# Optimization experiments

Measured on AMD Instinct MI355X. Metric: run time of the kernel, lower is better.

The kernel has to match this reference:

```python
import jax, jax.numpy as jnp
import numpy as np

B, L, EMB, U, V = 128, 64, 512, 1024, 50257
BN_EPS = 0.001


def setup_inputs() -> dict:
    key = jax.random.key(0)
    ks = jax.random.split(key, 20)
    s = 0.02
    return {
        "x": jax.random.randint(ks[0], (B, 1), 0, V, dtype=jnp.int64),
        "features": jax.random.normal(ks[1], (B, L, EMB), jnp.float32),
        "hidden": jax.random.normal(ks[2], (1, B, U), jnp.float32),
        "emb_table": jax.random.normal(ks[3], (V, EMB), jnp.float32) * s,
        "Uattn_w": jax.random.normal(ks[4], (U, EMB), jnp.float32) * s,
        "Uattn_b": jnp.zeros((U,), jnp.float32),
        "Wattn_w": jax.random.normal(ks[5], (U, U), jnp.float32) * s,
        "Wattn_b": jnp.zeros((U,), jnp.float32),
        "Vattn_w": jax.random.normal(ks[6], (1, U), jnp.float32) * s,
        "Vattn_b": jnp.zeros((1,), jnp.float32),
        "W_ih": jax.random.normal(ks[7], (3 * U, U), jnp.float32) * s,
        "W_hh": jax.random.normal(ks[8], (3 * U, U), jnp.float32) * s,
        "b_ih": jnp.zeros((3 * U,), jnp.float32),
        "b_hh": jnp.zeros((3 * U,), jnp.float32),
        "fc_w": jax.random.normal(ks[9], (U, U), jnp.float32) * s,
        "fc_b": jnp.zeros((U,), jnp.float32),
        "bn_gamma": jnp.ones((U,), jnp.float32),
        "bn_beta": jnp.zeros((U,), jnp.float32),
        "bn_mean": jnp.zeros((U,), jnp.float32),
        "bn_var": jnp.ones((U,), jnp.float32),
        "fc2_w": jax.random.normal(ks[10], (V, U), jnp.float32) * s,
        "fc2_b": jnp.zeros((V,), jnp.float32),
    }


def reference(x, features, hidden, emb_table, Uattn_w, Uattn_b, Wattn_w, Wattn_b,
              Vattn_w, Vattn_b, W_ih, W_hh, b_ih, b_hh, fc_w, fc_b,
              bn_gamma, bn_beta, bn_mean, bn_var, fc2_w, fc2_b):
    h = hidden[0]  # [B, U]
    # Bahdanau attention
    Uf = jnp.einsum('ble,ue->blu', features, Uattn_w) + Uattn_b        # [B,L,U]
    Wh = h @ Wattn_w.T + Wattn_b                                        # [B,U]
    score = jnp.tanh(Uf + Wh[:, None, :]) @ Vattn_w.T + Vattn_b        # [B,L,1]
    attn = jax.nn.softmax(score, axis=1)                                # [B,L,1]
    ctx = jnp.sum(attn * features, axis=1)                              # [B,EMB]
    # embed token and concat -> GRU input (seq len 1)
    e = emb_table[x[:, 0]]                                              # [B,EMB]
    gin = jnp.concatenate([ctx, e], axis=-1)                            # [B,U]
    # single-step GRU (PyTorch gate convention)
    gi = gin @ W_ih.T + b_ih                                            # [B,3U]
    gh = h @ W_hh.T + b_hh                                              # [B,3U]
    i_r, i_z, i_n = jnp.split(gi, 3, axis=-1)
    h_r, h_z, h_n = jnp.split(gh, 3, axis=-1)
    r = jax.nn.sigmoid(i_r + h_r)
    z = jax.nn.sigmoid(i_z + h_z)
    n = jnp.tanh(i_n + r * h_n)
    h_new = (1.0 - z) * n + z * h                                       # [B,U]
    # head: fc -> (dropout: identity in eval) -> BN (eval) -> fc2
    y = h_new @ fc_w.T + fc_b
    y = (y - bn_mean) * jax.lax.rsqrt(bn_var + BN_EPS) * bn_gamma + bn_beta
    logits = y @ fc2_w.T + fc2_b                                        # [B,V]
    return logits, h_new[None, :, :], attn
```

## Files before the change

### kernel.cpp

```cpp
#include <hip/hip_runtime.h>

typedef short bf8 __attribute__((ext_vector_type(8)));
typedef float f32x4 __attribute__((ext_vector_type(4)));

__device__ inline short f2bfs(float f) {
    unsigned u = __builtin_bit_cast(unsigned, f);
    u += 0x7FFFu + ((u >> 16) & 1u);
    return (short)(u >> 16);
}

__device__ inline unsigned pk2(float x, float y) {
    return (unsigned)(unsigned short)f2bfs(x) |
           ((unsigned)(unsigned short)f2bfs(y) << 16);
}

__device__ inline bf8 cvt_frag(f32x4 lo, f32x4 hi) {
    union { bf8 v; unsigned u[4]; } r;
    r.u[0] = pk2(lo[0], lo[1]);
    r.u[1] = pk2(lo[2], lo[3]);
    r.u[2] = pk2(hi[0], hi[1]);
    r.u[3] = pk2(hi[2], hi[3]);
    return r.v;
}

__device__ inline void gl_lds16(const void* g, void* l) {
    __builtin_amdgcn_global_load_lds(
        (const __attribute__((address_space(1))) unsigned int*)g,
        (__attribute__((address_space(3))) unsigned int*)l,
        16, 0, 0);
}

template<int EPI, int BM_, bool OBF>
__global__ __launch_bounds__(256) void gemm_bt(
    const short* __restrict__ A, const float* __restrict__ W,
    const float* __restrict__ bias, void* __restrict__ Cv,
    int M, int N, int K, int lda,
    const float* __restrict__ q0, const float* __restrict__ q1,
    const float* __restrict__ q2, const float* __restrict__ q3,
    float* __restrict__ score)
{
    constexpr int FM  = BM_ / 32;
    constexpr int ASZ = BM_ * 128;
    __shared__ __align__(1024) char smem[2 * ASZ + 32768];

    const int tid  = threadIdx.x;
    const int lane = tid & 63;
    const int wave = tid >> 6;
    const int wm0  = (wave >> 1) * (BM_ / 2);
    const int wn0  = (wave & 1) * 32;
    const int m0   = blockIdx.y * BM_;
    const int n0   = blockIdx.x * 64;

    f32x4 acc[FM][2] = {};

    auto stage = [&](int buf, int k0) {
        constexpr int APW = BM_ / 32;
        char* sA = smem + buf * ASZ;
        char* sW = smem + 2 * ASZ + buf * 16384;
        #pragma unroll
        for (int cc = 0; cc < APW; ++cc) {
            int c  = wave * APW + cc;
            int r  = c * 8 + (lane >> 3);
            int sl = (lane & 7) ^ (r & 7);
            gl_lds16(&A[(size_t)(m0 + r) * lda + k0 + sl * 8], sA + c * 1024);
        }
        #pragma unroll
        for (int cc = 0; cc < 4; ++cc) {
            int c  = wave * 4 + cc;
            int r  = c * 4 + (lane >> 4);
            int sl = (lane & 15) ^ (((r & 7) << 1) | ((r >> 3) & 1));
            int rg = n0 + r; rg = rg < N ? rg : N - 1;
            gl_lds16(&W[(size_t)rg * K + k0 + sl * 4], sW + c * 1024);
        }
    };

    auto compute = [&](int buf) {
        char* sA = smem + buf * ASZ;
        char* sW = smem + 2 * ASZ + buf * 16384;
        #pragma unroll
        for (int ks = 0; ks < 2; ++ks) {
            bf8 av[FM], bv[2];
            #pragma unroll
            for (int i = 0; i < FM; ++i) {
                int ra = wm0 + i * 16 + (lane & 15);
                int bc = ks * 64 + ((lane >> 4) * 16);
                av[i] = *reinterpret_cast<const bf8*>(
                    sA + ra * 128 + (bc ^ ((ra & 7) << 4)));
            }
            #pragma unroll
            for (int j = 0; j < 2; ++j) {
                int rb = wn0 + j * 16 + (lane & 15);
                int bl = ks * 128 + ((lane >> 4) * 32);
                int sw = ((rb & 7) << 5) | ((rb & 8) << 1);
                f32x4 lo = *reinterpret_cast<const f32x4*>(sW + rb * 256 + (bl ^ sw));
                f32x4 hi = *reinterpret_cast<const f32x4*>(sW + rb * 256 + ((bl + 16) ^ sw));
                bv[j] = cvt_frag(lo, hi);
            }
            #pragma unroll
            for (int i = 0; i < FM; ++i)
                #pragma unroll
                for (int j = 0; j < 2; ++j)
                    acc[i][j] = __builtin_amdgcn_mfma_f32_16x16x32_bf16(
                        av[i], bv[j], acc[i][j], 0, 0, 0);
        }
    };

    const int nt = K >> 6;
    int cur = 0;
    stage(0, 0);
    __syncthreads();
    for (int t = 0; t < nt - 1; ++t) {
        stage(cur ^ 1, (t + 1) << 6);
        compute(cur);
        __syncthreads();
        cur ^= 1;
    }
    compute(cur);

    if constexpr (EPI == 2) {
        #pragma unroll
        for (int i = 0; i < FM; ++i) {
            #pragma unroll
            for (int r = 0; r < 4; ++r) {
                int m = m0 + wm0 + i * 16 + (lane >> 4) * 4 + r;
                int bidx = m >> 6;
                float s = 0.f;
                #pragma unroll
                for (int j = 0; j < 2; ++j) {
                    int n = n0 + wn0 + j * 16 + (lane & 15);
                    s += tanhf(acc[i][j][r] + bias[n] + q0[(size_t)bidx * N + n]) * q1[n];
                }
                #pragma unroll
                for (int off = 1; off < 16; off <<= 1)
                    s += __shfl_xor(s, off);
                if ((lane & 15) == 0) atomicAdd(&score[m], s);
            }
        }
    } else {
        #pragma unroll
        for (int j = 0; j < 2; ++j) {
            int n = n0 + wn0 + j * 16 + (lane & 15);
            if (n >= N) continue;
            float bn_ = bias[n];
            float sc = 1.f, sh = 0.f;
            if constexpr (EPI == 1) {
                sc = q0[n] * rsqrtf(q3[n] + 1e-3f);
                sh = q1[n] - q2[n] * sc;
            }
            #pragma unroll
            for (int i = 0; i < FM; ++i) {
                #pragma unroll
                for (int r = 0; r < 4; ++r) {
                    int m = m0 + wm0 + i * 16 + (lane >> 4) * 4 + r;
                    float v = acc[i][j][r] + bn_;
                    if constexpr (EPI == 1) v = v * sc + sh;
                    if constexpr (OBF) ((short*)Cv)[(size_t)m * N + n] = f2bfs(v);
                    else               ((float*)Cv)[(size_t)m * N + n] = v;
                }
            }
        }
    }
}

__global__ __launch_bounds__(256) void cvt_bf16(
    const float* __restrict__ src, short* __restrict__ dst, int n8)
{
    for (int t = blockIdx.x * 256 + threadIdx.x; t < n8; t += gridDim.x * 256) {
        float4 v0 = *reinterpret_cast<const float4*>(src + (size_t)t * 8);
        float4 v1 = *reinterpret_cast<const float4*>(src + (size_t)t * 8 + 4);
        union { unsigned u[4]; uint4 q; } r;
        r.u[0] = pk2(v0.x, v0.y);
        r.u[1] = pk2(v0.z, v0.w);
        r.u[2] = pk2(v1.x, v1.y);
        r.u[3] = pk2(v1.z, v1.w);
        *reinterpret_cast<uint4*>(dst + (size_t)t * 8) = r.q;
    }
}

__global__ __launch_bounds__(256) void prep(
    const float* __restrict__ h, short* __restrict__ h_bf,
    float* __restrict__ score, const float* __restrict__ vb)
{
    int t = blockIdx.x * 256 + threadIdx.x;
    float4 v0 = *reinterpret_cast<const float4*>(h + (size_t)t * 8);
    float4 v1 = *reinterpret_cast<const float4*>(h + (size_t)t * 8 + 4);
    union { unsigned u[4]; uint4 q; } r;
    r.u[0] = pk2(v0.x, v0.y);
    r.u[1] = pk2(v0.z, v0.w);
    r.u[2] = pk2(v1.x, v1.y);
    r.u[3] = pk2(v1.z, v1.w);
    *reinterpret_cast<uint4*>(h_bf + (size_t)t * 8) = r.q;
    if (t < 1024) {
        float v = vb[0];
        float4 vv = make_float4(v, v, v, v);
        *reinterpret_cast<float4*>(score + t * 8)     = vv;
        *reinterpret_cast<float4*>(score + t * 8 + 4) = vv;
    }
}

__global__ __launch_bounds__(256) void softmax_ctx(
    const float* __restrict__ score, const float* __restrict__ features,
    const int* __restrict__ x, const float* __restrict__ emb,
    float* __restrict__ attn_out, short* __restrict__ gin_bf)
{
    int b = blockIdx.x;
    int t = threadIdx.x;
    __shared__ float sa[64];
    if (t < 64) {
        float v = score[b * 64 + t];
        float m = v;
        #pragma unroll
        for (int off = 32; off; off >>= 1) m = fmaxf(m, __shfl_xor(m, off));
        float e = expf(v - m);
        float s = e;
        #pragma unroll
        for (int off = 32; off; off >>= 1) s += __shfl_xor(s, off);
        float a = e / s;
        attn_out[b * 64 + t] = a;
        sa[t] = a;
    }
    __syncthreads();
    for (int e0 = t; e0 < 512; e0 += 256) {
        float c = 0.f;
        #pragma unroll 4
        for (int l = 0; l < 64; ++l)
            c += sa[l] * features[((size_t)b * 64 + l) * 512 + e0];
        gin_bf[(size_t)b * 1024 + e0] = f2bfs(c);
    }
    int xi = x[b];
    for (int e0 = t; e0 < 512; e0 += 256)
        gin_bf[(size_t)b * 1024 + 512 + e0] = f2bfs(emb[(size_t)xi * 512 + e0]);
}

__global__ __launch_bounds__(256) void gru_kernel(
    const float* __restrict__ gi, const float* __restrict__ gh,
    const float* __restrict__ h, float* __restrict__ hnew,
    short* __restrict__ hnew_bf)
{
    int idx = blockIdx.x * 256 + threadIdx.x;
    int b = idx >> 10, u = idx & 1023;
    const float* gib = gi + (size_t)b * 3072;
    const float* ghb = gh + (size_t)b * 3072;
    float ir = gib[u], iz = gib[1024 + u], in_ = gib[2048 + u];
    float hr = ghb[u], hz = ghb[1024 + u], hn = ghb[2048 + u];
    float r = 1.f / (1.f + expf(-(ir + hr)));
    float z = 1.f / (1.f + expf(-(iz + hz)));
    float n = tanhf(in_ + r * hn);
    float val = (1.f - z) * n + z * h[idx];
    hnew[idx] = val;
    hnew_bf[idx] = f2bfs(val);
}

extern "C" void kernel_launch(void* const* d_in, const int* in_sizes, int n_in,
                              void* d_out, int out_size, void* d_ws, size_t ws_size,
                              hipStream_t stream)
{
    const int*   x        = (const int*)  d_in[0];
    const float* features = (const float*)d_in[1];
    const float* hidden   = (const float*)d_in[2];
    const float* emb      = (const float*)d_in[3];
    const float* Uattn_w  = (const float*)d_in[4];
    const float* Uattn_b  = (const float*)d_in[5];
    const float* Wattn_w  = (const float*)d_in[6];
    const float* Wattn_b  = (const float*)d_in[7];
    const float* Vattn_w  = (const float*)d_in[8];
    const float* Vattn_b  = (const float*)d_in[9];
    const float* W_ih     = (const float*)d_in[10];
    const float* W_hh     = (const float*)d_in[11];
    const float* b_ih     = (const float*)d_in[12];
    const float* b_hh     = (const float*)d_in[13];
    const float* fc_w     = (const float*)d_in[14];
    const float* fc_b     = (const float*)d_in[15];
    const float* bn_gamma = (const float*)d_in[16];
    const float* bn_beta  = (const float*)d_in[17];
    const float* bn_mean  = (const float*)d_in[18];
    const float* bn_var   = (const float*)d_in[19];
    const float* fc2_w    = (const float*)d_in[20];
    const float* fc2_b    = (const float*)d_in[21];

    float* out    = (float*)d_out;
    float* logits = out;
    float* hnew   = out + 6432896;
    float* attn   = out + 6432896 + 131072;

    float* ws        = (float*)d_ws;
    float* Wh        = ws;
    float* scoreb    = ws + 131072;
    float* gi        = ws + 139264;
    float* gh        = ws + 532480;
    short* hidden_bf = (short*)(ws + 925696);
    short* gin_bf    = (short*)(ws + 991232);
    short* hnew_bf   = (short*)(ws + 1056768);
    short* y_bf      = (short*)(ws + 1122304);
    short* feat_bf   = (short*)(ws + 1187840);

    prep<<<64, 256, 0, stream>>>(hidden, hidden_bf, scoreb, Vattn_b);
    cvt_bf16<<<2048, 256, 0, stream>>>(features, feat_bf, 4194304 / 8);

    gemm_bt<0, 64, false><<<dim3(16, 2), 256, 0, stream>>>(
        hidden_bf, Wattn_w, Wattn_b, Wh, 128, 1024, 1024, 1024,
        nullptr, nullptr, nullptr, nullptr, nullptr);

    gemm_bt<2, 128, false><<<dim3(16, 64), 256, 0, stream>>>(
        feat_bf, Uattn_w, Uattn_b, nullptr, 8192, 1024, 512, 512,
        Wh, Vattn_w, nullptr, nullptr, scoreb);

    softmax_ctx<<<128, 256, 0, stream>>>(scoreb, features, x, emb, attn, gin_bf);

    gemm_bt<0, 64, false><<<dim3(48, 2), 256, 0, stream>>>(
        gin_bf, W_ih, b_ih, gi, 128, 3072, 1024, 1024,
        nullptr, nullptr, nullptr, nullptr, nullptr);
    gemm_bt<0, 64, false><<<dim3(48, 2), 256, 0, stream>>>(
        hidden_bf, W_hh, b_hh, gh, 128, 3072, 1024, 1024,
        nullptr, nullptr, nullptr, nullptr, nullptr);

    gru_kernel<<<512, 256, 0, stream>>>(gi, gh, hidden, hnew, hnew_bf);

    gemm_bt<1, 64, true><<<dim3(16, 2), 256, 0, stream>>>(
        hnew_bf, fc_w, fc_b, y_bf, 128, 1024, 1024, 1024,
        bn_gamma, bn_beta, bn_mean, bn_var, nullptr);

    gemm_bt<0, 128, false><<<dim3(786, 1), 256, 0, stream>>>(
        y_bf, fc2_w, fc2_b, logits, 128, 50257, 1024, 1024,
        nullptr, nullptr, nullptr, nullptr, nullptr);
}
```

Baseline: 175.4 us.

## Replace LDS-staged GEMM with direct register loads and merge small kernels

The GEMM drops its LDS double-buffering and syncthreads. Each wave now loads A fragments and fp32 W rows straight from global memory into registers, with a two-deep register prefetch, and always uses a 128-row M tile. Separately, the feature and hidden bf16 conversions are merged into one prep kernel, and the W_ih and W_hh GEMMs are merged into one launch via blockIdx.z. The softmax context sum now reads the bf16 features instead of fp32. Together these cut launch count, LDS traffic and barriers, at the risk of less coalesced global loads, no data sharing across waves (W rows are loaded redundantly by waves that share columns), and small grids for M=128 GEMMs with fewer blocks.

Result: slower. 305.3 us (+74.0%).

```diff
diff --git a/kernel.cpp b/kernel.cpp
--- a/kernel.cpp
+++ b/kernel.cpp
@@ -12,6 +12,11 @@
 __device__ inline unsigned pk2(float x, float y) {
     return (unsigned)(unsigned short)f2bfs(x) |
            ((unsigned)(unsigned short)f2bfs(y) << 16);
+}
+
+__device__ inline float bf2f(short s) {
+    unsigned u = ((unsigned)(unsigned short)s) << 16;
+    return __builtin_bit_cast(float, u);
 }
 
 __device__ inline bf8 cvt_frag(f32x4 lo, f32x4 hi) {
@@ -23,103 +28,78 @@
     return r.v;
 }
 
-__device__ inline void gl_lds16(const void* g, void* l) {
-    __builtin_amdgcn_global_load_lds(
-        (const __attribute__((address_space(1))) unsigned int*)g,
-        (__attribute__((address_space(3))) unsigned int*)l,
-        16, 0, 0);
-}
-
-template<int EPI, int BM_, bool OBF>
-__global__ __launch_bounds__(256) void gemm_bt(
+#define MFMA16 __builtin_amdgcn_mfma_f32_16x16x32_bf16
+
+template<int EPI, bool OBF>
+__device__ __forceinline__ void gemm_body(
     const short* __restrict__ A, const float* __restrict__ W,
     const float* __restrict__ bias, void* __restrict__ Cv,
-    int M, int N, int K, int lda,
+    int N, int K, int lda, int n0, int m0,
     const float* __restrict__ q0, const float* __restrict__ q1,
     const float* __restrict__ q2, const float* __restrict__ q3,
     float* __restrict__ score)
 {
-    constexpr int FM  = BM_ / 32;
-    constexpr int ASZ = BM_ * 128;
-    __shared__ __align__(1024) char smem[2 * ASZ + 32768];
-
-    const int tid  = threadIdx.x;
-    const int lane = tid & 63;
-    const int wave = tid >> 6;
-    const int wm0  = (wave >> 1) * (BM_ / 2);
+    const int lane = threadIdx.x & 63;
+    const int wave = threadIdx.x >> 6;
+    const int wm0  = (wave >> 1) * 64;
     const int wn0  = (wave & 1) * 32;
-    const int m0   = blockIdx.y * BM_;
-    const int n0   = blockIdx.x * 64;
-
-    f32x4 acc[FM][2] = {};
-
-    auto stage = [&](int buf, int k0) {
-        constexpr int APW = BM_ / 32;
-        char* sA = smem + buf * ASZ;
-        char* sW = smem + 2 * ASZ + buf * 16384;
-        #pragma unroll
-        for (int cc = 0; cc < APW; ++cc) {
-            int c  = wave * APW + cc;
-            int r  = c * 8 + (lane >> 3);
-            int sl = (lane & 7) ^ (r & 7);
-            gl_lds16(&A[(size_t)(m0 + r) * lda + k0 + sl * 8], sA + c * 1024);
-        }
-        #pragma unroll
-        for (int cc = 0; cc < 4; ++cc) {
-            int c  = wave * 4 + cc;
-            int r  = c * 4 + (lane >> 4);
-            int sl = (lane & 15) ^ (((r & 7) << 1) | ((r >> 3) & 1));
-            int rg = n0 + r; rg = rg < N ? rg : N - 1;
-            gl_lds16(&W[(size_t)rg * K + k0 + sl * 4], sW + c * 1024);
+    const int lr   = lane & 15;
+    const int lk8  = (lane >> 4) * 8;
+
+    f32x4 acc[4][2] = {};
+
+    const short* Ar0 = A + (size_t)(m0 + wm0 +  0 + lr) * lda + lk8;
+    const short* Ar1 = A + (size_t)(m0 + wm0 + 16 + lr) * lda + lk8;
+    const short* Ar2 = A + (size_t)(m0 + wm0 + 32 + lr) * lda + lk8;
+    const short* Ar3 = A + (size_t)(m0 + wm0 + 48 + lr) * lda + lk8;
+
+    int rb0 = n0 + wn0 + lr;       rb0 = rb0 < N ? rb0 : N - 1;
+    int rb1 = n0 + wn0 + 16 + lr;  rb1 = rb1 < N ? rb1 : N - 1;
+    const float* Wr0 = W + (size_t)rb0 * K + lk8;
+    const float* Wr1 = W + (size_t)rb1 * K + lk8;
+
+    auto loadW = [&](f32x4 (&dl)[2][2], f32x4 (&dh)[2][2], int ke) {
+        #pragma unroll
+        for (int ks = 0; ks < 2; ++ks) {
+            dl[ks][0] = *reinterpret_cast<const f32x4*>(Wr0 + ke + ks * 32);
+            dh[ks][0] = *reinterpret_cast<const f32x4*>(Wr0 + ke + ks * 32 + 4);
+            dl[ks][1] = *reinterpret_cast<const f32x4*>(Wr1 + ke + ks * 32);
+            dh[ks][1] = *reinterpret_cast<const f32x4*>(Wr1 + ke + ks * 32 + 4);
         }
     };
-
-    auto compute = [&](int buf) {
-        char* sA = smem + buf * ASZ;
-        char* sW = smem + 2 * ASZ + buf * 16384;
+    auto comp = [&](f32x4 (&sl)[2][2], f32x4 (&sh)[2][2], int ke) {
         #pragma unroll
         for (int ks = 0; ks < 2; ++ks) {
-            bf8 av[FM], bv[2];
-            #pragma unroll
-            for (int i = 0; i < FM; ++i) {
-                int ra = wm0 + i * 16 + (lane & 15);
-                int bc = ks * 64 + ((lane >> 4) * 16);
-                av[i] = *reinterpret_cast<const bf8*>(
-                    sA + ra * 128 + (bc ^ ((ra & 7) << 4)));
-            }
-            #pragma unroll
-            for (int j = 0; j < 2; ++j) {
-                int rb = wn0 + j * 16 + (lane & 15);
-                int bl = ks * 128 + ((lane >> 4) * 32);
-                int sw = ((rb & 7) << 5) | ((rb & 8) << 1);
-                f32x4 lo = *reinterpret_cast<const f32x4*>(sW + rb * 256 + (bl ^ sw));
-                f32x4 hi = *reinterpret_cast<const f32x4*>(sW + rb * 256 + ((bl + 16) ^ sw));
-                bv[j] = cvt_frag(lo, hi);
-            }
-            #pragma unroll
-            for (int i = 0; i < FM; ++i)
-                #pragma unroll
-                for (int j = 0; j < 2; ++j)
-                    acc[i][j] = __builtin_amdgcn_mfma_f32_16x16x32_bf16(
-                        av[i], bv[j], acc[i][j], 0, 0, 0);
+            bf8 a0 = *reinterpret_cast<const bf8*>(Ar0 + ke + ks * 32);
+            bf8 a1 = *reinterpret_cast<const bf8*>(Ar1 + ke + ks * 32);
+            bf8 a2 = *reinterpret_cast<const bf8*>(Ar2 + ke + ks * 32);
+            bf8 a3 = *reinterpret_cast<const bf8*>(Ar3 + ke + ks * 32);
+            bf8 b0 = cvt_frag(sl[ks][0], sh[ks][0]);
+            bf8 b1 = cvt_frag(sl[ks][1], sh[ks][1]);
+            acc[0][0] = MFMA16(a0, b0, acc[0][0], 0, 0, 0);
+            acc[0][1] = MFMA16(a0, b1, acc[0][1], 0, 0, 0);
+            acc[1][0] = MFMA16(a1, b0, acc[1][0], 0, 0, 0);
+            acc[1][1] = MFMA16(a1, b1, acc[1][1], 0, 0, 0);
+            acc[2][0] = MFMA16(a2, b0, acc[2][0], 0, 0, 0);
+            acc[2][1] = MFMA16(a2, b1, acc[2][1], 0, 0, 0);
+            acc[3][0] = MFMA16(a3, b0, acc[3][0], 0, 0, 0);
+            acc[3][1] = MFMA16(a3, b1, acc[3][1], 0, 0, 0);
         }
     };
 
+    f32x4 wl0[2][2], wh0[2][2], wl1[2][2], wh1[2][2];
     const int nt = K >> 6;
-    int cur = 0;
-    stage(0, 0);
-    __syncthreads();
-    for (int t = 0; t < nt - 1; ++t) {
-        stage(cur ^ 1, (t + 1) << 6);
-        compute(cur);
-        __syncthreads();
-        cur ^= 1;
-    }
-    compute(cur);
+    loadW(wl0, wh0, 0);
+    for (int t = 0; t < nt; t += 2) {
+        loadW(wl1, wh1, (t + 1) << 6);
+        comp(wl0, wh0, t << 6);
+        if (t + 2 < nt) loadW(wl0, wh0, (t + 2) << 6);
+        comp(wl1, wh1, (t + 1) << 6);
+    }
 
     if constexpr (EPI == 2) {
         #pragma unroll
-        for (int i = 0; i < FM; ++i) {
+        for (int i = 0; i < 4; ++i) {
             #pragma unroll
             for (int r = 0; r < 4; ++r) {
                 int m = m0 + wm0 + i * 16 + (lane >> 4) * 4 + r;
@@ -127,19 +107,19 @@
                 float s = 0.f;
                 #pragma unroll
                 for (int j = 0; j < 2; ++j) {
-                    int n = n0 + wn0 + j * 16 + (lane & 15);
+                    int n = n0 + wn0 + j * 16 + lr;
                     s += tanhf(acc[i][j][r] + bias[n] + q0[(size_t)bidx * N + n]) * q1[n];
                 }
                 #pragma unroll
                 for (int off = 1; off < 16; off <<= 1)
                     s += __shfl_xor(s, off);
-                if ((lane & 15) == 0) atomicAdd(&score[m], s);
+                if (lr == 0) atomicAdd(&score[m], s);
             }
         }
     } else {
         #pragma unroll
         for (int j = 0; j < 2; ++j) {
-            int n = n0 + wn0 + j * 16 + (lane & 15);
+            int n = n0 + wn0 + j * 16 + lr;
             if (n >= N) continue;
             float bn_ = bias[n];
             float sc = 1.f, sh = 0.f;
@@ -148,7 +128,7 @@
                 sh = q1[n] - q2[n] * sc;
             }
             #pragma unroll
-            for (int i = 0; i < FM; ++i) {
+            for (int i = 0; i < 4; ++i) {
                 #pragma unroll
                 for (int r = 0; r < 4; ++r) {
                     int m = m0 + wm0 + i * 16 + (lane >> 4) * 4 + r;
@@ -162,34 +142,54 @@
     }
 }
 
-__global__ __launch_bounds__(256) void cvt_bf16(
-    const float* __restrict__ src, short* __restrict__ dst, int n8)
-{
-    for (int t = blockIdx.x * 256 + threadIdx.x; t < n8; t += gridDim.x * 256) {
-        float4 v0 = *reinterpret_cast<const float4*>(src + (size_t)t * 8);
-        float4 v1 = *reinterpret_cast<const float4*>(src + (size_t)t * 8 + 4);
-        union { unsigned u[4]; uint4 q; } r;
-        r.u[0] = pk2(v0.x, v0.y);
-        r.u[1] = pk2(v0.z, v0.w);
-        r.u[2] = pk2(v1.x, v1.y);
-        r.u[3] = pk2(v1.z, v1.w);
-        *reinterpret_cast<uint4*>(dst + (size_t)t * 8) = r.q;
-    }
-}
-
-__global__ __launch_bounds__(256) void prep(
+template<int EPI, bool OBF>
+__global__ __launch_bounds__(256) void gemm_k(
+    const short* __restrict__ A, const float* __restrict__ W,
+    const float* __restrict__ bias, void* __restrict__ Cv,
+    int N, int K, int lda,
+    const float* __restrict__ q0, const float* __restrict__ q1,
+    const float* __restrict__ q2, const float* __restrict__ q3,
+    float* __restrict__ score)
+{
+    gemm_body<EPI, OBF>(A, W, bias, Cv, N, K, lda,
+                        blockIdx.x * 64, blockIdx.y * 128, q0, q1, q2, q3, score);
+}
+
+__global__ __launch_bounds__(256) void gemm_dual_k(
+    const short* __restrict__ A0, const float* __restrict__ W0,
+    const float* __restrict__ b0, float* __restrict__ C0,
+    const short* __restrict__ A1, const float* __restrict__ W1,
+    const float* __restrict__ b1, float* __restrict__ C1,
+    int N, int K, int lda)
+{
+    if (blockIdx.z == 0)
+        gemm_body<0, false>(A0, W0, b0, C0, N, K, lda, blockIdx.x * 64, 0,
+                            nullptr, nullptr, nullptr, nullptr, nullptr);
+    else
+        gemm_body<0, false>(A1, W1, b1, C1, N, K, lda, blockIdx.x * 64, 0,
+                            nullptr, nullptr, nullptr, nullptr, nullptr);
+}
+
+__global__ __launch_bounds__(256) void prep_all(
+    const float* __restrict__ feat, short* __restrict__ feat_bf,
     const float* __restrict__ h, short* __restrict__ h_bf,
     float* __restrict__ score, const float* __restrict__ vb)
 {
     int t = blockIdx.x * 256 + threadIdx.x;
-    float4 v0 = *reinterpret_cast<const float4*>(h + (size_t)t * 8);
-    float4 v1 = *reinterpret_cast<const float4*>(h + (size_t)t * 8 + 4);
-    union { unsigned u[4]; uint4 q; } r;
-    r.u[0] = pk2(v0.x, v0.y);
-    r.u[1] = pk2(v0.z, v0.w);
-    r.u[2] = pk2(v1.x, v1.y);
-    r.u[3] = pk2(v1.z, v1.w);
-    *reinterpret_cast<uint4*>(h_bf + (size_t)t * 8) = r.q;
+    {
+        float4 v0 = *reinterpret_cast<const float4*>(feat + (size_t)t * 8);
+        float4 v1 = *reinterpret_cast<const float4*>(feat + (size_t)t * 8 + 4);
+        uint4 q = make_uint4(pk2(v0.x, v0.y), pk2(v0.z, v0.w),
+                             pk2(v1.x, v1.y), pk2(v1.z, v1.w));
+        *reinterpret_cast<uint4*>(feat_bf + (size_t)t * 8) = q;
+    }
+    if (t < 16384) {
+        float4 v0 = *reinterpret_cast<const float4*>(h + (size_t)t * 8);
+        float4 v1 = *reinterpret_cast<const float4*>(h + (size_t)t * 8 + 4);
+        uint4 q = make_uint4(pk2(v0.x, v0.y), pk2(v0.z, v0.w),
+                             pk2(v1.x, v1.y), pk2(v1.z, v1.w));
+        *reinterpret_cast<uint4*>(h_bf + (size_t)t * 8) = q;
+    }
     if (t < 1024) {
         float v = vb[0];
         float4 vv = make_float4(v, v, v, v);
@@ -199,7 +199,7 @@
 }
 
 __global__ __launch_bounds__(256) void softmax_ctx(
-    const float* __restrict__ score, const float* __restrict__ features,
+    const float* __restrict__ score, const short* __restrict__ feat_bf,
     const int* __restrict__ x, const float* __restrict__ emb,
     float* __restrict__ attn_out, short* __restrict__ gin_bf)
 {
@@ -220,16 +220,25 @@
         sa[t] = a;
     }
     __syncthreads();
-    for (int e0 = t; e0 < 512; e0 += 256) {
-        float c = 0.f;
+    {
+        int e0 = t * 2;
+        float c0 = 0.f, c1 = 0.f;
         #pragma unroll 4
-        for (int l = 0; l < 64; ++l)
-            c += sa[l] * features[((size_t)b * 64 + l) * 512 + e0];
-        gin_bf[(size_t)b * 1024 + e0] = f2bfs(c);
-    }
-    int xi = x[b];
-    for (int e0 = t; e0 < 512; e0 += 256)
-        gin_bf[(size_t)b * 1024 + 512 + e0] = f2bfs(emb[(size_t)xi * 512 + e0]);
+        for (int l = 0; l < 64; ++l) {
+            float a = sa[l];
+            unsigned v = *reinterpret_cast<const unsigned*>(
+                &feat_bf[((size_t)b * 64 + l) * 512 + e0]);
+            c0 += a * bf2f((short)(v & 0xffff));
+            c1 += a * bf2f((short)(v >> 16));
+        }
+        *reinterpret_cast<unsigned*>(&gin_bf[(size_t)b * 1024 + e0]) = pk2(c0, c1);
+    }
+    {
+        int xi = x[b];
+        int e0 = t * 2;
+        float2 ev = *reinterpret_cast<const float2*>(&emb[(size_t)xi * 512 + e0]);
+        *reinterpret_cast<unsigned*>(&gin_bf[(size_t)b * 1024 + 512 + e0]) = pk2(ev.x, ev.y);
+    }
 }
 
 __global__ __launch_bounds__(256) void gru_kernel(
@@ -294,33 +303,30 @@
     short* y_bf      = (short*)(ws + 1122304);
     short* feat_bf   = (short*)(ws + 1187840);
 
-    prep<<<64, 256, 0, stream>>>(hidden, hidden_bf, scoreb, Vattn_b);
-    cvt_bf16<<<2048, 256, 0, stream>>>(features, feat_bf, 4194304 / 8);
-
-    gemm_bt<0, 64, false><<<dim3(16, 2), 256, 0, stream>>>(
-        hidden_bf, Wattn_w, Wattn_b, Wh, 128, 1024, 1024, 1024,
+    prep_all<<<2048, 256, 0, stream>>>(features, feat_bf, hidden, hidden_bf,
+                                       scoreb, Vattn_b);
+
+    gemm_k<0, false><<<dim3(16, 1), 256, 0, stream>>>(
+        hidden_bf, Wattn_w, Wattn_b, Wh, 1024, 1024, 1024,
         nullptr, nullptr, nullptr, nullptr, nullptr);
 
-    gemm_bt<2, 128, false><<<dim3(16, 64), 256, 0, stream>>>(
-        feat_bf, Uattn_w, Uattn_b, nullptr, 8192, 1024, 512, 512,
+    gemm_k<2, false><<<dim3(16, 64), 256, 0, stream>>>(
+        feat_bf, Uattn_w, Uattn_b, nullptr, 1024, 512, 512,
         Wh, Vattn_w, nullptr, nullptr, scoreb);
 
-    softmax_ctx<<<128, 256, 0, stream>>>(scoreb, features, x, emb, attn, gin_bf);
-
-    gemm_bt<0, 64, false><<<dim3(48, 2), 256, 0, stream>>>(
-        gin_bf, W_ih, b_ih, gi, 128, 3072, 1024, 1024,
+    softmax_ctx<<<128, 256, 0, stream>>>(scoreb, feat_bf, x, emb, attn, gin_bf);
+
+    gemm_dual_k<<<dim3(48, 1, 2), 256, 0, stream>>>(
+        gin_bf, W_ih, b_ih, gi,
+        hidden_bf, W_hh, b_hh, gh, 3072, 1024, 1024);
+
+    gru_kernel<<<512, 256, 0, stream>>>(gi, gh, hidden, hnew, hnew_bf);
+
+    gemm_k<1, true><<<dim3(16, 1), 256, 0, stream>>>(
+        hnew_bf, fc_w, fc_b, y_bf, 1024, 1024, 1024,
+        bn_gamma, bn_beta, bn_mean, bn_var, nullptr);
+
+    gemm_k<0, false><<<dim3(786, 1), 256, 0, stream>>>(
+        y_bf, fc2_w, fc2_b, logits, 50257, 1024, 1024,
         nullptr, nullptr, nullptr, nullptr, nullptr);
-    gemm_bt<0, 64, false><<<dim3(48, 2), 256, 0, stream>>>(
-        hidden_bf, W_hh, b_hh, gh, 128, 3072, 1024, 1024,
-        nullptr, nullptr, nullptr, nullptr, nullptr);
-
-    gru_kernel<<<512, 256, 0, stream>>>(gi, gh, hidden, hnew, hnew_bf);
-
-    gemm_bt<1, 64, true><<<dim3(16, 2), 256, 0, stream>>>(
-        hnew_bf, fc_w, fc_b, y_bf, 128, 1024, 1024, 1024,
-        bn_gamma, bn_beta, bn_mean, bn_var, nullptr);
-
-    gemm_bt<0, 128, false><<<dim3(786, 1), 256, 0, stream>>>(
-        y_bf, fc2_w, fc2_b, logits, 128, 50257, 1024, 1024,
-        nullptr, nullptr, nullptr, nullptr, nullptr);
-}
+}
```
